# Optimization experiments

Measured on AMD Instinct MI355X. Metric: run time of the kernel, lower is better.

The kernel has to match this reference:

```python
import jax, jax.numpy as jnp
import numpy as np

N, H = 8192, 1024

def setup_inputs() -> dict:
    key = jax.random.key(0)
    ks = jax.random.split(key, 7)
    s = 1.0 / np.sqrt(H)
    return {
        "input_tensor": jax.random.normal(ks[0], (N, H), dtype=jnp.float32),
        "Wq": jax.random.uniform(ks[1], (H, H), dtype=jnp.float32, minval=-s, maxval=s),
        "bq": jax.random.uniform(ks[2], (H,), dtype=jnp.float32, minval=-s, maxval=s),
        "Wk": jax.random.uniform(ks[3], (H, H), dtype=jnp.float32, minval=-s, maxval=s),
        "bk": jax.random.uniform(ks[4], (H,), dtype=jnp.float32, minval=-s, maxval=s),
        "Wv": jax.random.uniform(ks[5], (H, H), dtype=jnp.float32, minval=-s, maxval=s),
        "bv": jax.random.uniform(ks[6], (H,), dtype=jnp.float32, minval=-s, maxval=s),
    }

def reference(input_tensor, Wq, bq, Wk, bk, Wv, bv):
    # torch nn.Linear: x @ W.T + b
    q = input_tensor @ Wq.T + bq  # [N, H]
    k = input_tensor @ Wk.T + bk  # [N, H]
    v = input_tensor @ Wv.T + bv  # [N, H]
    scale = jnp.sqrt(jnp.asarray(input_tensor.shape[1], dtype=q.dtype))
    # (q @ k.T / sqrt(H)) @ v  -- no softmax; same math as original
    scores = (q @ k.T) / scale  # [N, N]
    return scores @ v  # [N, H]
```

## Files before the change

kernel.cpp:

```cpp
#include <hip/hip_runtime.h>
#include <hip/hip_bf16.h>
#include <stdint.h>
#include <stddef.h>

typedef __bf16 bf16_t;
typedef __bf16 bf16x4 __attribute__((ext_vector_type(4)));
typedef __bf16 bf16x8 __attribute__((ext_vector_type(8)));
typedef float  floatx4 __attribute__((ext_vector_type(4)));

#define TK 32

__global__ void prep_x(const float* __restrict__ x, bf16_t* __restrict__ xb,
                       bf16_t* __restrict__ xbT, float* __restrict__ s,
                       int SEQ, int H) {
    __shared__ bf16_t tile[64][72];
    __shared__ float csum[64];
    const int t = threadIdx.x;
    const int n0 = blockIdx.x * 64, k0 = blockIdx.y * 64;
    const int c4 = t & 15;
    const int rbase = t >> 4;
    float a0 = 0.f, a1 = 0.f, a2 = 0.f, a3 = 0.f;
    if (t < 64) csum[t] = 0.f;
    #pragma unroll
    for (int p = 0; p < 4; ++p) {
        const int r = rbase + 16 * p;
        const size_t gidx = (size_t)(n0 + r) * H + k0 + c4 * 4;
        float4 f = *(const float4*)(x + gidx);
        bf16x4 o;
        o.x = (bf16_t)f.x; o.y = (bf16_t)f.y;
        o.z = (bf16_t)f.z; o.w = (bf16_t)f.w;
        *(bf16x4*)(xb + gidx) = o;
        *(bf16x4*)&tile[r][c4 * 4] = o;
        a0 += f.x; a1 += f.y; a2 += f.z; a3 += f.w;
    }
    __syncthreads();
    atomicAdd(&csum[c4 * 4 + 0], a0);
    atomicAdd(&csum[c4 * 4 + 1], a1);
    atomicAdd(&csum[c4 * 4 + 2], a2);
    atomicAdd(&csum[c4 * 4 + 3], a3);
    #pragma unroll
    for (int p = 0; p < 2; ++p) {
        const int q = t + 256 * p;
        const int kk = q >> 3;
        const int n8 = (q & 7) * 8;
        bf16x8 v;
        #pragma unroll
        for (int u = 0; u < 8; ++u) v[u] = tile[n8 + u][kk];
        *(bf16x8*)(xbT + (size_t)(k0 + kk) * SEQ + n0 + n8) = v;
    }
    __syncthreads();
    if (t < 64) atomicAdd(s + k0 + t, csum[t]);
}

__global__ void prep_w(const float* __restrict__ Wk, bf16_t* __restrict__ Wkb,
                       const float* __restrict__ Wv, bf16_t* __restrict__ Wvb,
                       const float* __restrict__ Wq, bf16_t* __restrict__ WqTb,
                       float* __restrict__ svec) {
    __shared__ bf16_t tile[64][72];
    const int b = blockIdx.x;
    const int t = threadIdx.x;
    if (b == 2304) {
        *(float4*)(svec + t * 4) = float4{0.f, 0.f, 0.f, 0.f};
        return;
    }
    if (b < 2048) {
        const float* s = (b < 1024) ? Wk : Wv;
        bf16_t* d = (b < 1024) ? Wkb : Wvb;
        const int base = (b & 1023) * 1024 + t * 4;
        float4 f = *(const float4*)(s + base);
        bf16x4 o;
        o.x = (bf16_t)f.x; o.y = (bf16_t)f.y;
        o.z = (bf16_t)f.z; o.w = (bf16_t)f.w;
        *(bf16x4*)(d + base) = o;
    } else {
        const int bb = b - 2048;
        const int r0 = (bb & 15) * 64, c0 = (bb >> 4) * 64;
        const int c4 = t & 15;
        const int rbase = t >> 4;
        #pragma unroll
        for (int p = 0; p < 4; ++p) {
            const int r = rbase + 16 * p;
            float4 f = *(const float4*)(Wq + (size_t)(r0 + r) * 1024 + c0 + c4 * 4);
            bf16x4 o;
            o.x = (bf16_t)f.x; o.y = (bf16_t)f.y;
            o.z = (bf16_t)f.z; o.w = (bf16_t)f.w;
            *(bf16x4*)&tile[r][c4 * 4] = o;
        }
        __syncthreads();
        #pragma unroll
        for (int p = 0; p < 2; ++p) {
            const int q = t + 256 * p;
            const int cc = q >> 3;
            const int r8 = (q & 7) * 8;
            bf16x8 v;
            #pragma unroll
            for (int u = 0; u < 8; ++u) v[u] = tile[r8 + u][cc];
            *(bf16x8*)(WqTb + (size_t)(c0 + cc) * 1024 + r0 + r8) = v;
        }
    }
}

__global__ void matvec2(const bf16_t* __restrict__ M0,
                        const bf16_t* __restrict__ M1,
                        const float* __restrict__ v,
                        float* __restrict__ y0, float* __restrict__ y1,
                        int ncols) {
    const int lane = threadIdx.x & 63;
    const int row = blockIdx.x * 4 + (threadIdx.x >> 6);
    const bf16_t* mp;
    float* y;
    if (row < 1024) { mp = M0 + (size_t)row * ncols;          y = y0 + row; }
    else            { mp = M1 + (size_t)(row - 1024) * ncols; y = y1 + row - 1024; }
    float acc = 0.f;
    for (int a = lane * 8; a < ncols; a += 512) {
        bf16x8 m8 = *(const bf16x8*)(mp + a);
        #pragma unroll
        for (int u = 0; u < 8; ++u) acc += (float)m8[u] * v[a + u];
    }
    #pragma unroll
    for (int off = 32; off; off >>= 1) acc += __shfl_down(acc, off);
    if (lane == 0) *y = acc;
}

__global__ void matvec_bf16(const bf16_t* __restrict__ M,
                            const float* __restrict__ v,
                            float* __restrict__ y, int ncols, float scale) {
    const int lane = threadIdx.x & 63;
    const int row = blockIdx.x * 4 + (threadIdx.x >> 6);
    const bf16_t* mp = M + (size_t)row * ncols;
    float acc = 0.f;
    for (int a = lane * 8; a < ncols; a += 512) {
        bf16x8 m8 = *(const bf16x8*)(mp + a);
        #pragma unroll
        for (int u = 0; u < 8; ++u) acc += (float)m8[u] * v[a + u];
    }
    #pragma unroll
    for (int off = 32; off; off >>= 1) acc += __shfl_down(acc, off);
    if (lane == 0) y[row] = acc * scale;
}

__global__ void reduce_bf16(const bf16_t* __restrict__ part,
                            bf16_t* __restrict__ dst, int n, int nsplit,
                            float scale) {
    int i = (blockIdx.x * blockDim.x + threadIdx.x) * 8;
    if (i < n) {
        float acc[8] = {};
        for (int z = 0; z < nsplit; ++z) {
            bf16x8 p = *(const bf16x8*)(part + (size_t)z * n + i);
            #pragma unroll
            for (int u = 0; u < 8; ++u) acc[u] += (float)p[u];
        }
        bf16x8 o;
        #pragma unroll
        for (int u = 0; u < 8; ++u) o[u] = (bf16_t)(acc[u] * scale);
        *(bf16x8*)(dst + i) = o;
    }
}

__global__ void reduce_bf16_rank1(const bf16_t* __restrict__ part,
                                  bf16_t* __restrict__ dst, int n, int nsplit,
                                  const float* __restrict__ bv,
                                  const float* __restrict__ kv1,
                                  const float* __restrict__ wvs,
                                  const float* __restrict__ bk,
                                  float cN, int Hdim) {
    int i = (blockIdx.x * blockDim.x + threadIdx.x) * 8;
    if (i < n) {
        float acc[8] = {};
        for (int z = 0; z < nsplit; ++z) {
            bf16x8 p = *(const bf16x8*)(part + (size_t)z * n + i);
            #pragma unroll
            for (int u = 0; u < 8; ++u) acc[u] += (float)p[u];
        }
        const int j = i / Hdim, ii = i % Hdim;
        const float bvj = bv[j], wvsj = wvs[j];
        bf16x8 o;
        #pragma unroll
        for (int u = 0; u < 8; ++u) {
            float v = acc[u] + bvj * kv1[ii + u] + (wvsj + cN * bvj) * bk[ii + u];
            o[u] = (bf16_t)v;
        }
        *(bf16x8*)(dst + i) = o;
    }
}

template <int TMp, int TNp, int MODE, int SWZ, typename OutT>
__global__ __launch_bounds__(256, 2) void gemm_bt(
    const bf16_t* __restrict__ A,
    const bf16_t* __restrict__ B,
    OutT* __restrict__ C,
    const float* __restrict__ p1,
    int M, int N, int K, int kChunk, float scale)
{
    __shared__ __align__(16) bf16_t As[TMp * TK];
    __shared__ __align__(16) bf16_t Bs[TNp * TK];
    constexpr int MF = TMp / 32;
    constexpr int NF = TNp / 32;
    constexpr int nA = TMp / 64;
    constexpr int nB = TNp / 64;

    const int tid  = threadIdx.x;
    const int lane = tid & 63;
    const int wave = tid >> 6;
    const int wm   = wave >> 1;
    const int wn   = wave & 1;

    int bm, bn, z;
    if (SWZ == 0) {
        bm = blockIdx.y * TMp; bn = blockIdx.x * TNp; z = blockIdx.z;
    } else if (SWZ == 1) {
        const int L = blockIdx.x;
        z = ((L & 7) << 1) | (L >> 9);
        const int mn = (L >> 3) & 63;
        bm = (mn >> 3) * TMp; bn = (mn & 7) * TNp;
    } else if (SWZ == 2) {
        const int L = blockIdx.x;
        bm = ((L & 7) * 8 + ((L >> 3) & 7)) * TMp;
        bn = (L >> 6) * TNp;
        z = 0;
    } else {
        const int L = blockIdx.x;
        z = L & 7;
        const int mn = L >> 3;
        bm = (mn >> 3) * TMp; bn = (mn & 7) * TNp;
    }
    const int k0 = z * kChunk;
    C += (size_t)z * M * N;

    floatx4 acc[MF][NF] = {};

    const int fr = lane & 15;
    const int fk = (lane >> 4) * 8;

    for (int kt = k0; kt < k0 + kChunk; kt += TK) {
        #pragma unroll
        for (int p = 0; p < nA; ++p) {
            const int c = tid + 256 * p;
            const int r = c >> 2, o = (c & 3) * 8;
            __builtin_amdgcn_global_load_lds(
                (const __attribute__((address_space(1))) void*)
                    (A + (size_t)(bm + r) * K + kt + o),
                (__attribute__((address_space(3))) void*)&As[c * 8], 16, 0, 0);
        }
        #pragma unroll
        for (int p = 0; p < nB; ++p) {
            const int c = tid + 256 * p;
            const int r = c >> 2, o = (c & 3) * 8;
            __builtin_amdgcn_global_load_lds(
                (const __attribute__((address_space(1))) void*)
                    (B + (size_t)(bn + r) * K + kt + o),
                (__attribute__((address_space(3))) void*)&Bs[c * 8], 16, 0, 0);
        }
        __syncthreads();

        bf16x8 af[MF], bg[NF];
        #pragma unroll
        for (int i = 0; i < MF; ++i)
            af[i] = *(const bf16x8*)&As[(wm * (TMp / 2) + i * 16 + fr) * TK + fk];
        #pragma unroll
        for (int j = 0; j < NF; ++j)
            bg[j] = *(const bf16x8*)&Bs[(wn * (TNp / 2) + j * 16 + fr) * TK + fk];
        #pragma unroll
        for (int i = 0; i < MF; ++i) {
            #pragma unroll
            for (int j = 0; j < NF; ++j) {
                acc[i][j] = __builtin_amdgcn_mfma_f32_16x16x32_bf16(
                    af[i], bg[j], acc[i][j], 0, 0, 0);
            }
        }
        __syncthreads();
    }

    const int rq = (lane >> 4) * 4;
    #pragma unroll
    for (int i = 0; i < MF; ++i) {
        #pragma unroll
        for (int j = 0; j < NF; ++j) {
            const int col = bn + wn * (TNp / 2) + j * 16 + fr;
            #pragma unroll
            for (int r = 0; r < 4; ++r) {
                const int row = bm + wm * (TMp / 2) + i * 16 + rq + r;
                float v = acc[i][j][r] * scale;
                if (MODE == 1) v += p1[col];
                C[(size_t)row * N + col] = (OutT)v;
            }
        }
    }
}

extern "C" void kernel_launch(void* const* d_in, const int* in_sizes, int n_in,
                              void* d_out, int out_size, void* d_ws, size_t ws_size,
                              hipStream_t stream) {
    const int SEQ = 8192;
    const int H   = 1024;

    const float* x  = (const float*)d_in[0];
    const float* Wq = (const float*)d_in[1];
    const float* bq = (const float*)d_in[2];
    const float* Wk = (const float*)d_in[3];
    const float* bk = (const float*)d_in[4];
    const float* Wv = (const float*)d_in[5];
    const float* bv = (const float*)d_in[6];
    float* out = (float*)d_out;

    const size_t MI = 1024 * 1024;
    char* ws = (char*)d_ws;
    bf16_t* xb   = (bf16_t*)(ws);
    bf16_t* xbT  = (bf16_t*)(ws + 16 * MI);
    bf16_t* Wkb  = (bf16_t*)(ws + 32 * MI);
    bf16_t* Wvb  = (bf16_t*)(ws + 34 * MI);
    bf16_t* WqTb = (bf16_t*)(ws + 36 * MI);
    bf16_t* Gb   = (bf16_t*)(ws + 38 * MI);
    bf16_t* S1b  = (bf16_t*)(ws + 40 * MI);
    bf16_t* Ttb  = (bf16_t*)(ws + 42 * MI);
    bf16_t* Utb  = (bf16_t*)(ws + 44 * MI);
    float*  svec = (float*)(ws + 46 * MI);
    float*  kv1  = svec + 1024;
    float*  wvs  = svec + 2048;
    float*  cvec = svec + 3072;
    bf16_t* part = (bf16_t*)(ws + 48 * MI);

    dim3 blk(256);
    const float inv32 = 1.0f / 32.0f;
    const int nHH = H * H;
    const int rgrid = nHH / 8 / 256;
    const float* nil = nullptr;

    prep_w<<<dim3(2305), blk, 0, stream>>>(Wk, Wkb, Wv, Wvb, Wq, WqTb, svec);
    prep_x<<<dim3(SEQ / 64, H / 64), blk, 0, stream>>>(x, xb, xbT, svec, SEQ, H);
    matvec2<<<dim3(512), blk, 0, stream>>>(Wkb, Wvb, svec, kv1, wvs, H);
    gemm_bt<128, 128, 0, 1, bf16_t><<<dim3(1024), blk, 0, stream>>>(
        xbT, xbT, part, nil, H, H, SEQ, SEQ / 16, 1.0f);
    reduce_bf16<<<dim3(rgrid), blk, 0, stream>>>(part, Gb, nHH, 16, 1.0f);
    gemm_bt<128, 128, 0, 3, bf16_t><<<dim3(512), blk, 0, stream>>>(
        Wvb, Gb, part, nil, H, H, H, H / 8, 1.0f);
    reduce_bf16<<<dim3(rgrid), blk, 0, stream>>>(part, S1b, nHH, 8, 1.0f);
    gemm_bt<128, 128, 0, 3, bf16_t><<<dim3(512), blk, 0, stream>>>(
        S1b, Wkb, part, nil, H, H, H, H / 8, 1.0f);
    reduce_bf16_rank1<<<dim3(rgrid), blk, 0, stream>>>(
        part, Ttb, nHH, 8, bv, kv1, wvs, bk, (float)SEQ, H);
    matvec_bf16<<<dim3(H / 4), blk, 0, stream>>>(Ttb, bq, cvec, H, inv32);
    gemm_bt<128, 128, 0, 3, bf16_t><<<dim3(512), blk, 0, stream>>>(
        Ttb, WqTb, part, nil, H, H, H, H / 8, 1.0f);
    reduce_bf16<<<dim3(rgrid), blk, 0, stream>>>(part, Utb, nHH, 8, inv32);
    gemm_bt<128, 128, 1, 2, float><<<dim3(512), blk, 0, stream>>>(
        xb, Utb, out, cvec, SEQ, H, H, H, 1.0f);
}
```

Baseline: 230.5 us.

## Fuse split-K reductions and matvecs into GEMM launches via last-block counters

Adds a gemm_red kernel that writes its split-K partials, then uses a per-tile atomic counter so the last-arriving block sums all partials and writes the reduced bf16 output. That last block also applies the scale or the rank-1 bias correction. The separate matvec kernels run as extra blocks appended to the GEMM grids, and prep_w zeroes the counters each call. The aim is to remove several kernel launches and their serialization gaps. In exchange it adds threadfence and atomic overhead, a serial reduction tail inside each tile, and a simpler single-buffered GEMM main loop.

```diff
diff --git a/kernel.cpp b/kernel.cpp
--- a/kernel.cpp
+++ b/kernel.cpp
@@ -55,12 +55,13 @@
 __global__ void prep_w(const float* __restrict__ Wk, bf16_t* __restrict__ Wkb,
                        const float* __restrict__ Wv, bf16_t* __restrict__ Wvb,
                        const float* __restrict__ Wq, bf16_t* __restrict__ WqTb,
-                       float* __restrict__ svec) {
+                       float* __restrict__ svec, int* __restrict__ cnt) {
     __shared__ bf16_t tile[64][72];
     const int b = blockIdx.x;
     const int t = threadIdx.x;
     if (b == 2304) {
         *(float4*)(svec + t * 4) = float4{0.f, 0.f, 0.f, 0.f};
+        if (t < 64) ((int4*)cnt)[t] = int4{0, 0, 0, 0};
         return;
     }
     if (b < 2048) {
@@ -100,87 +101,154 @@
     }
 }
 
-__global__ void matvec2(const bf16_t* __restrict__ M0,
-                        const bf16_t* __restrict__ M1,
-                        const float* __restrict__ v,
-                        float* __restrict__ y0, float* __restrict__ y1,
-                        int ncols) {
-    const int lane = threadIdx.x & 63;
-    const int row = blockIdx.x * 4 + (threadIdx.x >> 6);
-    const bf16_t* mp;
-    float* y;
-    if (row < 1024) { mp = M0 + (size_t)row * ncols;          y = y0 + row; }
-    else            { mp = M1 + (size_t)(row - 1024) * ncols; y = y1 + row - 1024; }
-    float acc = 0.f;
-    for (int a = lane * 8; a < ncols; a += 512) {
-        bf16x8 m8 = *(const bf16x8*)(mp + a);
-        #pragma unroll
-        for (int u = 0; u < 8; ++u) acc += (float)m8[u] * v[a + u];
-    }
+template <int RED, int MERGE, int NS, int SWZ>
+__global__ __launch_bounds__(256, 2) void gemm_red(
+    const bf16_t* __restrict__ A, const bf16_t* __restrict__ B,
+    bf16_t* __restrict__ part, bf16_t* __restrict__ dst,
+    int* __restrict__ cnt, int M, int N, int K, int kChunk, float scaleR,
+    const float* __restrict__ e_bv, const float* __restrict__ e_kv1,
+    const float* __restrict__ e_wvs, const float* __restrict__ e_bk, float cN,
+    const bf16_t* __restrict__ mvM0, const bf16_t* __restrict__ mvM1,
+    const float* __restrict__ mvv, float* __restrict__ mvy0,
+    float* __restrict__ mvy1, float mvScale)
+{
+    constexpr int NGEMM = 64 * NS;
+    const int L = blockIdx.x;
+    const int tid = threadIdx.x;
+
+    if (MERGE && L >= NGEMM) {
+        const int lane = tid & 63, wv = tid >> 6;
+        const int nr = (MERGE == 1) ? 2 : 1;
+        #pragma unroll
+        for (int rr = 0; rr < ((MERGE == 1) ? 2 : 1); ++rr) {
+            const int row = (L - NGEMM) * 4 * nr + wv * nr + rr;
+            const bf16_t* mp;
+            float* y;
+            if (MERGE == 1 && row >= 1024) {
+                mp = mvM1 + (size_t)(row - 1024) * 1024;
+                y = mvy1 + row - 1024;
+            } else {
+                mp = mvM0 + (size_t)row * 1024;
+                y = mvy0 + row;
+            }
+            float acc = 0.f;
+            for (int a = lane * 8; a < 1024; a += 512) {
+                bf16x8 m8 = *(const bf16x8*)(mp + a);
+                #pragma unroll
+                for (int u = 0; u < 8; ++u) acc += (float)m8[u] * mvv[a + u];
+            }
+            #pragma unroll
+            for (int off = 32; off; off >>= 1) acc += __shfl_down(acc, off);
+            if (lane == 0) *y = acc * mvScale;
+        }
+        return;
+    }
+
+    __shared__ __align__(16) bf16_t As[128 * TK];
+    __shared__ __align__(16) bf16_t Bs[128 * TK];
+    constexpr int MF = 4;
+    constexpr int NF = 4;
+    const int lane = tid & 63;
+    const int wave = tid >> 6;
+    const int wm = wave >> 1;
+    const int wn = wave & 1;
+
+    int mn, z;
+    if (SWZ == 1) { z = ((L & 7) << 1) | (L >> 9); mn = (L >> 3) & 63; }
+    else          { z = L & 7;                     mn = L >> 3; }
+    const int bm = (mn >> 3) * 128, bn = (mn & 7) * 128;
+    const int k0 = z * kChunk;
+    bf16_t* C = part + (size_t)z * M * N;
+
+    floatx4 acc[MF][NF] = {};
+    const int fr = lane & 15;
+    const int fk = (lane >> 4) * 8;
+
+    for (int kt = k0; kt < k0 + kChunk; kt += TK) {
+        #pragma unroll
+        for (int p = 0; p < 2; ++p) {
+            const int c = tid + 256 * p;
+            const int r = c >> 2, o = (c & 3) * 8;
+            __builtin_amdgcn_global_load_lds(
+                (const __attribute__((address_space(1))) void*)
+                    (A + (size_t)(bm + r) * K + kt + o),
+                (__attribute__((address_space(3))) void*)&As[c * 8], 16, 0, 0);
+        }
+        #pragma unroll
+        for (int p = 0; p < 2; ++p) {
+            const int c = tid + 256 * p;
+            const int r = c >> 2, o = (c & 3) * 8;
+            __builtin_amdgcn_global_load_lds(
+                (const __attribute__((address_space(1))) void*)
+                    (B + (size_t)(bn + r) * K + kt + o),
+                (__attribute__((address_space(3))) void*)&Bs[c * 8], 16, 0, 0);
+        }
+        __syncthreads();
+
+        bf16x8 af[MF], bg[NF];
+        #pragma unroll
+        for (int i = 0; i < MF; ++i)
+            af[i] = *(const bf16x8*)&As[(wm * 64 + i * 16 + fr) * TK + fk];
+        #pragma unroll
+        for (int j = 0; j < NF; ++j)
+            bg[j] = *(const bf16x8*)&Bs[(wn * 64 + j * 16 + fr) * TK + fk];
+        #pragma unroll
+        for (int i = 0; i < MF; ++i) {
+            #pragma unroll
+            for (int j = 0; j < NF; ++j) {
+                acc[i][j] = __builtin_amdgcn_mfma_f32_16x16x32_bf16(
+                    af[i], bg[j], acc[i][j], 0, 0, 0);
+            }
+        }
+        __syncthreads();
+    }
+
+    const int rq = (lane >> 4) * 4;
     #pragma unroll
-    for (int off = 32; off; off >>= 1) acc += __shfl_down(acc, off);
-    if (lane == 0) *y = acc;
-}
-
-__global__ void matvec_bf16(const bf16_t* __restrict__ M,
-                            const float* __restrict__ v,
-                            float* __restrict__ y, int ncols, float scale) {
-    const int lane = threadIdx.x & 63;
-    const int row = blockIdx.x * 4 + (threadIdx.x >> 6);
-    const bf16_t* mp = M + (size_t)row * ncols;
-    float acc = 0.f;
-    for (int a = lane * 8; a < ncols; a += 512) {
-        bf16x8 m8 = *(const bf16x8*)(mp + a);
-        #pragma unroll
-        for (int u = 0; u < 8; ++u) acc += (float)m8[u] * v[a + u];
-    }
+    for (int i = 0; i < MF; ++i) {
+        #pragma unroll
+        for (int j = 0; j < NF; ++j) {
+            const int col = bn + wn * 64 + j * 16 + fr;
+            #pragma unroll
+            for (int r = 0; r < 4; ++r) {
+                const int row = bm + wm * 64 + i * 16 + rq + r;
+                C[(size_t)row * N + col] = (bf16_t)acc[i][j][r];
+            }
+        }
+    }
+
+    __threadfence();
+    __syncthreads();
+    __shared__ int sLast;
+    if (tid == 0) sLast = (atomicAdd(cnt + mn, 1) == NS - 1);
+    __syncthreads();
+    if (!sLast) return;
+    __threadfence();
+
+    const int cc = (tid & 15) * 8;
+    const int r0 = tid >> 4;
     #pragma unroll
-    for (int off = 32; off; off >>= 1) acc += __shfl_down(acc, off);
-    if (lane == 0) y[row] = acc * scale;
-}
-
-__global__ void reduce_bf16(const bf16_t* __restrict__ part,
-                            bf16_t* __restrict__ dst, int n, int nsplit,
-                            float scale) {
-    int i = (blockIdx.x * blockDim.x + threadIdx.x) * 8;
-    if (i < n) {
-        float acc[8] = {};
-        for (int z = 0; z < nsplit; ++z) {
-            bf16x8 p = *(const bf16x8*)(part + (size_t)z * n + i);
-            #pragma unroll
-            for (int u = 0; u < 8; ++u) acc[u] += (float)p[u];
+    for (int ru = 0; ru < 8; ++ru) {
+        const int row = bm + r0 + ru * 16;
+        const size_t off = (size_t)row * N + bn + cc;
+        float a8[8] = {};
+        for (int zz = 0; zz < NS; ++zz) {
+            bf16x8 p = *(const bf16x8*)(part + (size_t)zz * M * N + off);
+            #pragma unroll
+            for (int u = 0; u < 8; ++u) a8[u] += (float)p[u];
         }
         bf16x8 o;
-        #pragma unroll
-        for (int u = 0; u < 8; ++u) o[u] = (bf16_t)(acc[u] * scale);
-        *(bf16x8*)(dst + i) = o;
-    }
-}
-
-__global__ void reduce_bf16_rank1(const bf16_t* __restrict__ part,
-                                  bf16_t* __restrict__ dst, int n, int nsplit,
-                                  const float* __restrict__ bv,
-                                  const float* __restrict__ kv1,
-                                  const float* __restrict__ wvs,
-                                  const float* __restrict__ bk,
-                                  float cN, int Hdim) {
-    int i = (blockIdx.x * blockDim.x + threadIdx.x) * 8;
-    if (i < n) {
-        float acc[8] = {};
-        for (int z = 0; z < nsplit; ++z) {
-            bf16x8 p = *(const bf16x8*)(part + (size_t)z * n + i);
-            #pragma unroll
-            for (int u = 0; u < 8; ++u) acc[u] += (float)p[u];
-        }
-        const int j = i / Hdim, ii = i % Hdim;
-        const float bvj = bv[j], wvsj = wvs[j];
-        bf16x8 o;
-        #pragma unroll
-        for (int u = 0; u < 8; ++u) {
-            float v = acc[u] + bvj * kv1[ii + u] + (wvsj + cN * bvj) * bk[ii + u];
-            o[u] = (bf16_t)v;
-        }
-        *(bf16x8*)(dst + i) = o;
+        if (RED == 2) {
+            const float bvj = e_bv[row];
+            const float w = e_wvs[row] + cN * bvj;
+            #pragma unroll
+            for (int u = 0; u < 8; ++u)
+                o[u] = (bf16_t)(a8[u] + bvj * e_kv1[bn + cc + u] + w * e_bk[bn + cc + u]);
+        } else {
+            #pragma unroll
+            for (int u = 0; u < 8; ++u) o[u] = (bf16_t)(a8[u] * scaleR);
+        }
+        *(bf16x8*)(dst + off) = o;
     }
 }
 
@@ -208,11 +276,6 @@
     int bm, bn, z;
     if (SWZ == 0) {
         bm = blockIdx.y * TMp; bn = blockIdx.x * TNp; z = blockIdx.z;
-    } else if (SWZ == 1) {
-        const int L = blockIdx.x;
-        z = ((L & 7) << 1) | (L >> 9);
-        const int mn = (L >> 3) & 63;
-        bm = (mn >> 3) * TMp; bn = (mn & 7) * TNp;
     } else if (SWZ == 2) {
         const int L = blockIdx.x;
         bm = ((L & 7) * 8 + ((L >> 3) & 7)) * TMp;
@@ -318,31 +381,29 @@
     float*  kv1  = svec + 1024;
     float*  wvs  = svec + 2048;
     float*  cvec = svec + 3072;
+    int*    cnt  = (int*)(svec + 4096);
     bf16_t* part = (bf16_t*)(ws + 48 * MI);
 
     dim3 blk(256);
     const float inv32 = 1.0f / 32.0f;
-    const int nHH = H * H;
-    const int rgrid = nHH / 8 / 256;
-    const float* nil = nullptr;
-
-    prep_w<<<dim3(2305), blk, 0, stream>>>(Wk, Wkb, Wv, Wvb, Wq, WqTb, svec);
+    const float* nf = nullptr;
+    const bf16_t* nb = nullptr;
+    float* nfm = nullptr;
+
+    prep_w<<<dim3(2305), blk, 0, stream>>>(Wk, Wkb, Wv, Wvb, Wq, WqTb, svec, cnt);
     prep_x<<<dim3(SEQ / 64, H / 64), blk, 0, stream>>>(x, xb, xbT, svec, SEQ, H);
-    matvec2<<<dim3(512), blk, 0, stream>>>(Wkb, Wvb, svec, kv1, wvs, H);
-    gemm_bt<128, 128, 0, 1, bf16_t><<<dim3(1024), blk, 0, stream>>>(
-        xbT, xbT, part, nil, H, H, SEQ, SEQ / 16, 1.0f);
-    reduce_bf16<<<dim3(rgrid), blk, 0, stream>>>(part, Gb, nHH, 16, 1.0f);
-    gemm_bt<128, 128, 0, 3, bf16_t><<<dim3(512), blk, 0, stream>>>(
-        Wvb, Gb, part, nil, H, H, H, H / 8, 1.0f);
-    reduce_bf16<<<dim3(rgrid), blk, 0, stream>>>(part, S1b, nHH, 8, 1.0f);
-    gemm_bt<128, 128, 0, 3, bf16_t><<<dim3(512), blk, 0, stream>>>(
-        S1b, Wkb, part, nil, H, H, H, H / 8, 1.0f);
-    reduce_bf16_rank1<<<dim3(rgrid), blk, 0, stream>>>(
-        part, Ttb, nHH, 8, bv, kv1, wvs, bk, (float)SEQ, H);
-    matvec_bf16<<<dim3(H / 4), blk, 0, stream>>>(Ttb, bq, cvec, H, inv32);
-    gemm_bt<128, 128, 0, 3, bf16_t><<<dim3(512), blk, 0, stream>>>(
-        Ttb, WqTb, part, nil, H, H, H, H / 8, 1.0f);
-    reduce_bf16<<<dim3(rgrid), blk, 0, stream>>>(part, Utb, nHH, 8, inv32);
+    gemm_red<1, 1, 16, 1><<<dim3(1280), blk, 0, stream>>>(
+        xbT, xbT, part, Gb, cnt + 0, H, H, SEQ, SEQ / 16, 1.0f,
+        nf, nf, nf, nf, 0.f, Wkb, Wvb, svec, kv1, wvs, 1.0f);
+    gemm_red<1, 0, 8, 3><<<dim3(512), blk, 0, stream>>>(
+        Wvb, Gb, part, S1b, cnt + 64, H, H, H, H / 8, 1.0f,
+        nf, nf, nf, nf, 0.f, nb, nb, nf, nfm, nfm, 0.f);
+    gemm_red<2, 0, 8, 3><<<dim3(512), blk, 0, stream>>>(
+        S1b, Wkb, part, Ttb, cnt + 128, H, H, H, H / 8, 1.0f,
+        bv, kv1, wvs, bk, (float)SEQ, nb, nb, nf, nfm, nfm, 0.f);
+    gemm_red<1, 2, 8, 3><<<dim3(768), blk, 0, stream>>>(
+        Ttb, WqTb, part, Utb, cnt + 192, H, H, H, H / 8, inv32,
+        nf, nf, nf, nf, 0.f, Ttb, nb, bq, cvec, nfm, inv32);
     gemm_bt<128, 128, 1, 2, float><<<dim3(512), blk, 0, stream>>>(
         xb, Utb, out, cvec, SEQ, H, H, H, 1.0f);
 }
```

After: 795.6 us. 245% more time.

## Fold matvecs into GEMM launches and drop split-K for 1024x1024 GEMMs

Applied to the files above, without the earlier changes.

Appends extra blocks to the Gram and Ttb@WqT GEMM launches that compute the matvecs previously run as separate kernels. The three HxH GEMMs switch from split-K (8-way) with a separate reduction kernel to full-K 64x64 tiles that write bf16 results directly. The rank-1 bias correction moves into the GEMM epilogue. This removes several launches and the partial-buffer traffic, but each GEMM now has only 256 blocks with a long K loop, so parallelism per block drops.

```diff
diff --git a/kernel.cpp b/kernel.cpp
--- a/kernel.cpp
+++ b/kernel.cpp
@@ -100,45 +100,6 @@
     }
 }
 
-__global__ void matvec2(const bf16_t* __restrict__ M0,
-                        const bf16_t* __restrict__ M1,
-                        const float* __restrict__ v,
-                        float* __restrict__ y0, float* __restrict__ y1,
-                        int ncols) {
-    const int lane = threadIdx.x & 63;
-    const int row = blockIdx.x * 4 + (threadIdx.x >> 6);
-    const bf16_t* mp;
-    float* y;
-    if (row < 1024) { mp = M0 + (size_t)row * ncols;          y = y0 + row; }
-    else            { mp = M1 + (size_t)(row - 1024) * ncols; y = y1 + row - 1024; }
-    float acc = 0.f;
-    for (int a = lane * 8; a < ncols; a += 512) {
-        bf16x8 m8 = *(const bf16x8*)(mp + a);
-        #pragma unroll
-        for (int u = 0; u < 8; ++u) acc += (float)m8[u] * v[a + u];
-    }
-    #pragma unroll
-    for (int off = 32; off; off >>= 1) acc += __shfl_down(acc, off);
-    if (lane == 0) *y = acc;
-}
-
-__global__ void matvec_bf16(const bf16_t* __restrict__ M,
-                            const float* __restrict__ v,
-                            float* __restrict__ y, int ncols, float scale) {
-    const int lane = threadIdx.x & 63;
-    const int row = blockIdx.x * 4 + (threadIdx.x >> 6);
-    const bf16_t* mp = M + (size_t)row * ncols;
-    float acc = 0.f;
-    for (int a = lane * 8; a < ncols; a += 512) {
-        bf16x8 m8 = *(const bf16x8*)(mp + a);
-        #pragma unroll
-        for (int u = 0; u < 8; ++u) acc += (float)m8[u] * v[a + u];
-    }
-    #pragma unroll
-    for (int off = 32; off; off >>= 1) acc += __shfl_down(acc, off);
-    if (lane == 0) y[row] = acc * scale;
-}
-
 __global__ void reduce_bf16(const bf16_t* __restrict__ part,
                             bf16_t* __restrict__ dst, int n, int nsplit,
                             float scale) {
@@ -157,41 +118,48 @@
     }
 }
 
-__global__ void reduce_bf16_rank1(const bf16_t* __restrict__ part,
-                                  bf16_t* __restrict__ dst, int n, int nsplit,
-                                  const float* __restrict__ bv,
-                                  const float* __restrict__ kv1,
-                                  const float* __restrict__ wvs,
-                                  const float* __restrict__ bk,
-                                  float cN, int Hdim) {
-    int i = (blockIdx.x * blockDim.x + threadIdx.x) * 8;
-    if (i < n) {
-        float acc[8] = {};
-        for (int z = 0; z < nsplit; ++z) {
-            bf16x8 p = *(const bf16x8*)(part + (size_t)z * n + i);
-            #pragma unroll
-            for (int u = 0; u < 8; ++u) acc[u] += (float)p[u];
-        }
-        const int j = i / Hdim, ii = i % Hdim;
-        const float bvj = bv[j], wvsj = wvs[j];
-        bf16x8 o;
-        #pragma unroll
-        for (int u = 0; u < 8; ++u) {
-            float v = acc[u] + bvj * kv1[ii + u] + (wvsj + cN * bvj) * bk[ii + u];
-            o[u] = (bf16_t)v;
-        }
-        *(bf16x8*)(dst + i) = o;
-    }
-}
-
-template <int TMp, int TNp, int MODE, int SWZ, typename OutT>
+template <int TMp, int TNp, int MODE, int SWZ, int MERGE, typename OutT>
 __global__ __launch_bounds__(256, 2) void gemm_bt(
-    const bf16_t* __restrict__ A,
-    const bf16_t* __restrict__ B,
-    OutT* __restrict__ C,
-    const float* __restrict__ p1,
-    int M, int N, int K, int kChunk, float scale)
+    const bf16_t* __restrict__ A, const bf16_t* __restrict__ B,
+    OutT* __restrict__ C, const float* __restrict__ p1,
+    int M, int N, int K, int kChunk, float scale, int ngemm,
+    const float* __restrict__ e_bv, const float* __restrict__ e_kv1,
+    const float* __restrict__ e_wvs, const float* __restrict__ e_bk, float cN,
+    const bf16_t* __restrict__ mvM0, const bf16_t* __restrict__ mvM1,
+    const float* __restrict__ mvv, float* __restrict__ mvy0,
+    float* __restrict__ mvy1, float mvScale)
 {
+    const int tid = threadIdx.x;
+    const int L = blockIdx.x;
+
+    if (MERGE && L >= ngemm) {
+        const int lane = tid & 63, wv = tid >> 6;
+        #pragma unroll
+        for (int rr = 0; rr < ((MERGE == 1) ? 2 : 1); ++rr) {
+            const bf16_t* mp;
+            float* y;
+            if (MERGE == 1) {
+                const int row = (L - ngemm) * 8 + wv * 2 + rr;
+                if (row >= 1024) { mp = mvM1 + (size_t)(row - 1024) * 1024; y = mvy1 + row - 1024; }
+                else             { mp = mvM0 + (size_t)row * 1024;          y = mvy0 + row; }
+            } else {
+                const int row = (L - ngemm) * 4 + wv;
+                mp = mvM0 + (size_t)row * 1024;
+                y = mvy0 + row;
+            }
+            float acc = 0.f;
+            for (int a = lane * 8; a < 1024; a += 512) {
+                bf16x8 m8 = *(const bf16x8*)(mp + a);
+                #pragma unroll
+                for (int u = 0; u < 8; ++u) acc += (float)m8[u] * mvv[a + u];
+            }
+            #pragma unroll
+            for (int off = 32; off; off >>= 1) acc += __shfl_down(acc, off);
+            if (lane == 0) *y = acc * mvScale;
+        }
+        return;
+    }
+
     __shared__ __align__(16) bf16_t As[TMp * TK];
     __shared__ __align__(16) bf16_t Bs[TNp * TK];
     constexpr int MF = TMp / 32;
@@ -199,36 +167,29 @@
     constexpr int nA = TMp / 64;
     constexpr int nB = TNp / 64;
 
-    const int tid  = threadIdx.x;
     const int lane = tid & 63;
     const int wave = tid >> 6;
     const int wm   = wave >> 1;
     const int wn   = wave & 1;
 
     int bm, bn, z;
-    if (SWZ == 0) {
-        bm = blockIdx.y * TMp; bn = blockIdx.x * TNp; z = blockIdx.z;
-    } else if (SWZ == 1) {
-        const int L = blockIdx.x;
+    if (SWZ == 1) {
         z = ((L & 7) << 1) | (L >> 9);
         const int mn = (L >> 3) & 63;
         bm = (mn >> 3) * TMp; bn = (mn & 7) * TNp;
     } else if (SWZ == 2) {
-        const int L = blockIdx.x;
         bm = ((L & 7) * 8 + ((L >> 3) & 7)) * TMp;
         bn = (L >> 6) * TNp;
         z = 0;
     } else {
-        const int L = blockIdx.x;
-        z = L & 7;
-        const int mn = L >> 3;
-        bm = (mn >> 3) * TMp; bn = (mn & 7) * TNp;
+        bm = (L >> 4) * TMp;
+        bn = (L & 15) * TNp;
+        z = 0;
     }
     const int k0 = z * kChunk;
     C += (size_t)z * M * N;
 
     floatx4 acc[MF][NF] = {};
-
     const int fr = lane & 15;
     const int fk = (lane >> 4) * 8;
 
@@ -282,6 +243,8 @@
                 const int row = bm + wm * (TMp / 2) + i * 16 + rq + r;
                 float v = acc[i][j][r] * scale;
                 if (MODE == 1) v += p1[col];
+                if (MODE == 2)
+                    v += e_bv[row] * e_kv1[col] + (e_wvs[row] + cN * e_bv[row]) * e_bk[col];
                 C[(size_t)row * N + col] = (OutT)v;
             }
         }
@@ -324,25 +287,26 @@
     const float inv32 = 1.0f / 32.0f;
     const int nHH = H * H;
     const int rgrid = nHH / 8 / 256;
-    const float* nil = nullptr;
+    const float* nf = nullptr;
+    const bf16_t* nb = nullptr;
+    float* nfm = nullptr;
 
     prep_w<<<dim3(2305), blk, 0, stream>>>(Wk, Wkb, Wv, Wvb, Wq, WqTb, svec);
     prep_x<<<dim3(SEQ / 64, H / 64), blk, 0, stream>>>(x, xb, xbT, svec, SEQ, H);
-    matvec2<<<dim3(512), blk, 0, stream>>>(Wkb, Wvb, svec, kv1, wvs, H);
-    gemm_bt<128, 128, 0, 1, bf16_t><<<dim3(1024), blk, 0, stream>>>(
-        xbT, xbT, part, nil, H, H, SEQ, SEQ / 16, 1.0f);
+    gemm_bt<128, 128, 0, 1, 1, bf16_t><<<dim3(1280), blk, 0, stream>>>(
+        xbT, xbT, part, nf, H, H, SEQ, SEQ / 16, 1.0f, 1024,
+        nf, nf, nf, nf, 0.f, Wkb, Wvb, svec, kv1, wvs, 1.0f);
     reduce_bf16<<<dim3(rgrid), blk, 0, stream>>>(part, Gb, nHH, 16, 1.0f);
-    gemm_bt<128, 128, 0, 3, bf16_t><<<dim3(512), blk, 0, stream>>>(
-        Wvb, Gb, part, nil, H, H, H, H / 8, 1.0f);
-    reduce_bf16<<<dim3(rgrid), blk, 0, stream>>>(part, S1b, nHH, 8, 1.0f);
-    gemm_bt<128, 128, 0, 3, bf16_t><<<dim3(512), blk, 0, stream>>>(
-        S1b, Wkb, part, nil, H, H, H, H / 8, 1.0f);
-    reduce_bf16_rank1<<<dim3(rgrid), blk, 0, stream>>>(
-        part, Ttb, nHH, 8, bv, kv1, wvs, bk, (float)SEQ, H);
-    matvec_bf16<<<dim3(H / 4), blk, 0, stream>>>(Ttb, bq, cvec, H, inv32);
-    gemm_bt<128, 128, 0, 3, bf16_t><<<dim3(512), blk, 0, stream>>>(
-        Ttb, WqTb, part, nil, H, H, H, H / 8, 1.0f);
-    reduce_bf16<<<dim3(rgrid), blk, 0, stream>>>(part, Utb, nHH, 8, inv32);
-    gemm_bt<128, 128, 1, 2, float><<<dim3(512), blk, 0, stream>>>(
-        xb, Utb, out, cvec, SEQ, H, H, H, 1.0f);
-}
+    gemm_bt<64, 64, 0, 4, 0, bf16_t><<<dim3(256), blk, 0, stream>>>(
+        Wvb, Gb, S1b, nf, H, H, H, H, 1.0f, 1 << 30,
+        nf, nf, nf, nf, 0.f, nb, nb, nf, nfm, nfm, 0.f);
+    gemm_bt<64, 64, 2, 4, 0, bf16_t><<<dim3(256), blk, 0, stream>>>(
+        S1b, Wkb, Ttb, nf, H, H, H, H, 1.0f, 1 << 30,
+        bv, kv1, wvs, bk, (float)SEQ, nb, nb, nf, nfm, nfm, 0.f);
+    gemm_bt<64, 64, 0, 4, 2, bf16_t><<<dim3(512), blk, 0, stream>>>(
+        Ttb, WqTb, Utb, nf, H, H, H, H, inv32, 256,
+        nf, nf, nf, nf, 0.f, Ttb, nb, bq, cvec, nfm, inv32);
+    gemm_bt<128, 128, 1, 2, 0, float><<<dim3(512), blk, 0, stream>>>(
+        xb, Utb, out, cvec, SEQ, H, H, H, 1.0f, 1 << 30,
+        nf, nf, nf, nf, 0.f, nb, nb, nf, nfm, nfm, 0.f);
+}
```

New measurement: 212.0 us. -8.0%, faster.
